# Kernel tuning notes

Hardware: AMD Instinct MI355X
Metric: run time of the kernel (lower is better)

## Reference

```python
import jax, jax.numpy as jnp
import numpy as np

B, S = 4096, 256
D = 32  # output_size // 4


def setup_inputs() -> dict:
    key = jax.random.key(0)
    ks = jax.random.split(key, 32)
    # continuous features
    cont_p = jax.random.normal(ks[0], (B, S, 3), dtype=jnp.float32)
    cont_c = jax.random.normal(ks[1], (B, S, 2), dtype=jnp.float32)
    # categorical features, per-column vocab sizes from Embedding tables
    vocabs_p = [2, 2, 2, 11, 34]
    cat_p = jnp.stack([
        jax.random.randint(ks[2 + i], (B, S), 0, v, dtype=jnp.int32)
        for i, v in enumerate(vocabs_p)], axis=2)
    vocabs_c = [19, 31]
    cat_c = jnp.stack([
        jax.random.randint(ks[7 + i], (B, S), 0, v, dtype=jnp.int32)
        for i, v in enumerate(vocabs_c)], axis=2)
    lengths = jax.random.randint(ks[9], (B,), 1, S + 1, dtype=jnp.int32)

    def lin(k, fan_in, fan_out):
        bound = 1.0 / np.sqrt(fan_in)
        kw, kb = jax.random.split(k)
        w = jax.random.uniform(kw, (fan_in, fan_out), jnp.float32, -bound, bound)
        b = jax.random.uniform(kb, (fan_out,), jnp.float32, -bound, bound)
        return w, b

    w_p1, b_p1 = lin(ks[10], 3, D)
    w_p2, b_p2 = lin(ks[11], D, D)
    w_c1, b_c1 = lin(ks[12], 2, D)
    w_c2, b_c2 = lin(ks[13], D, D)
    emb_gender = jax.random.normal(ks[14], (2, D), dtype=jnp.float32)
    emb_korean = jax.random.normal(ks[15], (2, D), dtype=jnp.float32)
    emb_primary = jax.random.normal(ks[16], (2, D), dtype=jnp.float32)
    emb_job = jax.random.normal(ks[17], (11, D), dtype=jnp.float32)
    emb_rep = jax.random.normal(ks[18], (34, D), dtype=jnp.float32)
    emb_place = jax.random.normal(ks[19], (19, D), dtype=jnp.float32)
    emb_add = jax.random.normal(ks[20], (31, D), dtype=jnp.float32)
    w_fc1, b_fc1 = lin(ks[21], 128, 64)
    w_fc2, b_fc2 = lin(ks[22], 64, 2)

    return dict(cont_p=cont_p, cont_c=cont_c, cat_p=cat_p, cat_c=cat_c,
                lengths=lengths,
                w_p1=w_p1, b_p1=b_p1, w_p2=w_p2, b_p2=b_p2,
                w_c1=w_c1, b_c1=b_c1, w_c2=w_c2, b_c2=b_c2,
                emb_gender=emb_gender, emb_korean=emb_korean,
                emb_primary=emb_primary, emb_job=emb_job, emb_rep=emb_rep,
                emb_place=emb_place, emb_add=emb_add,
                w_fc1=w_fc1, b_fc1=b_fc1, w_fc2=w_fc2, b_fc2=b_fc2)


def reference(cont_p, cont_c, cat_p, cat_c, lengths,
              w_p1, b_p1, w_p2, b_p2, w_c1, b_c1, w_c2, b_c2,
              emb_gender, emb_korean, emb_primary, emb_job, emb_rep,
              emb_place, emb_add, w_fc1, b_fc1, w_fc2, b_fc2):
    # small per-token MLPs on continuous features -> [B,S,D]
    hp = jax.nn.relu(cont_p @ w_p1 + b_p1) @ w_p2 + b_p2
    hc = jax.nn.relu(cont_c @ w_c1 + b_c1) @ w_c2 + b_c2
    # multi-table embedding lookups, averaged per group -> [B,S,D]
    ep = (emb_gender[cat_p[:, :, 0]] + emb_korean[cat_p[:, :, 1]] +
          emb_primary[cat_p[:, :, 2]] + emb_job[cat_p[:, :, 3]] +
          emb_rep[cat_p[:, :, 4]]) / 5.0
    ec = (emb_place[cat_c[:, :, 0]] + emb_add[cat_c[:, :, 1]]) / 2.0
    # concat order matches torch: (cat_p, cat_c, cont_p, cont_c) -> [B,S,128]
    x = jnp.concatenate([ep, ec, hp, hc], axis=2)
    # ragged mean pool over first lengths[i] positions (masked segment mean)
    mask = (jnp.arange(x.shape[1])[None, :] < lengths[:, None])
    pooled = jnp.sum(x * mask[:, :, None], axis=1) / lengths[:, None].astype(x.dtype)
    # head: relu(fc1) -> relu(fc2); dropout p=0.0 is identity
    h = jax.nn.relu(pooled @ w_fc1 + b_fc1)
    return jax.nn.relu(h @ w_fc2 + b_fc2)
```

## Files before the change

### kernel.cpp

```cpp
#include <hip/hip_runtime.h>


#define BDIM 64

__global__ __launch_bounds__(BDIM)
void mlpreg_kernel(const float* __restrict__ cont_p,
                   const float* __restrict__ cont_c,
                   const int* __restrict__ cat_p,
                   const int* __restrict__ cat_c,
                   const int* __restrict__ lengths,
                   const float* __restrict__ w_p1, const float* __restrict__ b_p1,
                   const float* __restrict__ w_p2, const float* __restrict__ b_p2,
                   const float* __restrict__ w_c1, const float* __restrict__ b_c1,
                   const float* __restrict__ w_c2, const float* __restrict__ b_c2,
                   const float* __restrict__ emb_g,  const float* __restrict__ emb_k,
                   const float* __restrict__ emb_pr, const float* __restrict__ emb_j,
                   const float* __restrict__ emb_r,  const float* __restrict__ emb_pl,
                   const float* __restrict__ emb_a,
                   const float* __restrict__ w_fc1, const float* __restrict__ b_fc1,
                   const float* __restrict__ w_fc2, const float* __restrict__ b_fc2,
                   float* __restrict__ out)
{
    constexpr int S = 256;
    __shared__ float sP4[S * 4];
    __shared__ float sC2[S * 2];
    __shared__ int   hist[96];
    __shared__ float sPacc[64];
    __shared__ float sPooled[128];

    const int lane = threadIdx.x;
    const int b    = blockIdx.x;
    int L = lengths[b];
    if (L < 1) L = 1;
    if (L > S) L = S;
    const float invL = 1.0f / (float)L;
    const float Lf   = (float)L;

    const int*   kp = cat_p  + (size_t)b * (S * 5);
    const int*   kc = cat_c  + (size_t)b * (S * 2);
    const float* gp = cont_p + (size_t)b * (S * 3);
    const float* gc = cont_c + (size_t)b * (S * 2);

    hist[lane] = 0;
    if (lane < 32) hist[64 + lane] = 0;
    __syncthreads();

    for (int t = lane; t < L; t += BDIM) {
        float c0 = gp[t * 3 + 0], c1 = gp[t * 3 + 1], c2 = gp[t * 3 + 2];
        float4 v; v.x = c0; v.y = c1; v.z = c2; v.w = 0.f;
        *(float4*)&sP4[t * 4] = v;
        float2 u = *(const float2*)(gc + t * 2);
        *(float2*)&sC2[t * 2] = u;
    }

    int sg = 0, sk = 0, spr = 0;
    for (int i = lane; i < 5 * L; i += BDIM) {
        int v = kp[i];
        int col = i % 5;
        if      (col == 0) sg  += v;
        else if (col == 1) sk  += v;
        else if (col == 2) spr += v;
        else if (col == 3) atomicAdd(&hist[v], 1);
        else               atomicAdd(&hist[11 + v], 1);
    }
    for (int i = lane; i < 2 * L; i += BDIM) {
        int v = kc[i];
        atomicAdd(&hist[(i & 1) ? (64 + v) : (45 + v)], 1);
    }
    #pragma unroll
    for (int d = 32; d; d >>= 1) {
        sg  += __shfl_xor(sg,  d);
        sk  += __shfl_xor(sk,  d);
        spr += __shfl_xor(spr, d);
    }
    __syncthreads();

    const int pr = lane >> 5, ch = lane & 31;
    const float wp0 = w_p1[ch], wp1 = w_p1[32 + ch], wp2 = w_p1[64 + ch], bp = b_p1[ch];
    const float wc0 = w_c1[ch], wc1 = w_c1[32 + ch], bc = b_c1[ch];

    float accP = 0.f, accC = 0.f;
    #pragma unroll 4
    for (int t = pr; t < L; t += 2) {
        float4 cp = *(const float4*)&sP4[t * 4];
        float2 cc = *(const float2*)&sC2[t * 2];
        accP += fmaxf(fmaf(cp.x, wp0, fmaf(cp.y, wp1, fmaf(cp.z, wp2, bp))), 0.f);
        accC += fmaxf(fmaf(cc.x, wc0, fmaf(cc.y, wc1, bc)), 0.f);
    }
    accP += __shfl_down(accP, 32);
    accC += __shfl_down(accC, 32);
    if (lane < 32) {
        sPacc[ch]      = accP * invL;
        sPacc[32 + ch] = accC * invL;
    }

    if (pr == 0) {
        float cg = (float)sg, ck = (float)sk, cp = (float)spr;
        float s0 = fmaf(Lf - cg, emb_g[ch],  fmaf(cg, emb_g[32 + ch],
                   fmaf(Lf - ck, emb_k[ch],  ck * emb_k[32 + ch])));
        float s1 = fmaf(Lf - cp, emb_pr[ch], cp * emb_pr[32 + ch]);
        #pragma unroll
        for (int r = 0; r < 11; ++r) s0 = fmaf((float)hist[r],      emb_j[r * 32 + ch], s0);
        #pragma unroll
        for (int r = 0; r < 34; r += 2) {
            s0 = fmaf((float)hist[11 + r],     emb_r[(r + 0) * 32 + ch], s0);
            s1 = fmaf((float)hist[11 + r + 1], emb_r[(r + 1) * 32 + ch], s1);
        }
        sPooled[ch] = (s0 + s1) * (invL * 0.2f);
    } else {
        float s0 = 0.f, s1 = 0.f;
        #pragma unroll
        for (int r = 0; r < 19; ++r) s0 = fmaf((float)hist[45 + r], emb_pl[r * 32 + ch], s0);
        #pragma unroll
        for (int r = 0; r < 31; r += 2) {
            s0 = fmaf((float)hist[64 + r], emb_a[(r + 0) * 32 + ch], s0);
            if (r + 1 < 31)
                s1 = fmaf((float)hist[64 + r + 1], emb_a[(r + 1) * 32 + ch], s1);
        }
        sPooled[32 + ch] = (s0 + s1) * (invL * 0.5f);
    }
    __syncthreads();

    if (pr == 0) {
        float v0 = b_p2[ch], v1 = 0.f;
        #pragma unroll
        for (int k = 0; k < 32; k += 2) {
            v0 = fmaf(sPacc[k],     w_p2[(k + 0) * 32 + ch], v0);
            v1 = fmaf(sPacc[k + 1], w_p2[(k + 1) * 32 + ch], v1);
        }
        sPooled[64 + ch] = v0 + v1;
    } else {
        float v0 = b_c2[ch], v1 = 0.f;
        #pragma unroll
        for (int k = 0; k < 32; k += 2) {
            v0 = fmaf(sPacc[32 + k],     w_c2[(k + 0) * 32 + ch], v0);
            v1 = fmaf(sPacc[32 + k + 1], w_c2[(k + 1) * 32 + ch], v1);
        }
        sPooled[96 + ch] = v0 + v1;
    }
    __syncthreads();

    const float* wk = w_fc1 + lane;
    float v0 = b_fc1[lane], v1 = 0.f, v2 = 0.f, v3 = 0.f;
    #pragma unroll 8
    for (int k = 0; k < 128; k += 4) {
        float4 x = *(const float4*)&sPooled[k];
        v0 = fmaf(x.x, wk[(size_t)(k + 0) * 64], v0);
        v1 = fmaf(x.y, wk[(size_t)(k + 1) * 64], v1);
        v2 = fmaf(x.z, wk[(size_t)(k + 2) * 64], v2);
        v3 = fmaf(x.w, wk[(size_t)(k + 3) * 64], v3);
    }
    float h = fmaxf((v0 + v1) + (v2 + v3), 0.f);

    float p0 = h * w_fc2[lane * 2 + 0];
    float p1 = h * w_fc2[lane * 2 + 1];
    #pragma unroll
    for (int d = 32; d; d >>= 1) {
        p0 += __shfl_xor(p0, d);
        p1 += __shfl_xor(p1, d);
    }
    if (lane == 0) {
        float2 o;
        o.x = fmaxf(p0 + b_fc2[0], 0.f);
        o.y = fmaxf(p1 + b_fc2[1], 0.f);
        *(float2*)&out[(size_t)b * 2] = o;
    }
}

extern "C" void kernel_launch(void* const* d_in, const int* in_sizes, int n_in,
                              void* d_out, int out_size, void* d_ws, size_t ws_size,
                              hipStream_t stream) {
    const float* cont_p = (const float*)d_in[0];
    const float* cont_c = (const float*)d_in[1];
    const int*   cat_p  = (const int*)d_in[2];
    const int*   cat_c  = (const int*)d_in[3];
    const int*   lens   = (const int*)d_in[4];
    const float* w_p1   = (const float*)d_in[5];
    const float* b_p1   = (const float*)d_in[6];
    const float* w_p2   = (const float*)d_in[7];
    const float* b_p2   = (const float*)d_in[8];
    const float* w_c1   = (const float*)d_in[9];
    const float* b_c1   = (const float*)d_in[10];
    const float* w_c2   = (const float*)d_in[11];
    const float* b_c2   = (const float*)d_in[12];
    const float* emb_g  = (const float*)d_in[13];
    const float* emb_k  = (const float*)d_in[14];
    const float* emb_pr = (const float*)d_in[15];
    const float* emb_j  = (const float*)d_in[16];
    const float* emb_r  = (const float*)d_in[17];
    const float* emb_pl = (const float*)d_in[18];
    const float* emb_a  = (const float*)d_in[19];
    const float* w_fc1  = (const float*)d_in[20];
    const float* b_fc1  = (const float*)d_in[21];
    const float* w_fc2  = (const float*)d_in[22];
    const float* b_fc2  = (const float*)d_in[23];
    float* out = (float*)d_out;

    const int B = 4096;
    hipLaunchKernelGGL(mlpreg_kernel, dim3(B), dim3(BDIM), 0, stream,
                       cont_p, cont_c, cat_p, cat_c, lens,
                       w_p1, b_p1, w_p2, b_p2, w_c1, b_c1, w_c2, b_c2,
                       emb_g, emb_k, emb_pr, emb_j, emb_r, emb_pl, emb_a,
                       w_fc1, b_fc1, w_fc2, b_fc2, out);
}
```

Before: 144.9 us.

## Compute per-token MLP in registers per lane and reduce across the wave with transposed shuffles

Each lane now owns up to four tokens and accumulates all 32 hidden channels of both first-layer MLPs in registers. A butterfly transpose-reduce across the wave then produces the per-channel pooled sums. This replaces the shared-memory staging of continuous features and one barrier. Categorical columns are read per token in a single pass: the three binary columns are packed into one integer for the shuffle reduction, and all histogram updates are merged into one loop. The aim is to expose more independent memory loads and cut shared-memory round trips, at the cost of many more live registers and redundant weight loads per lane.

```diff
diff --git a/kernel.cpp b/kernel.cpp
--- a/kernel.cpp
+++ b/kernel.cpp
@@ -3,7 +3,67 @@
 
 #define BDIM 64
 
-__global__ __launch_bounds__(BDIM)
+__device__ __forceinline__ float wave_sum64(float v) {
+    #pragma unroll
+    for (int d = 32; d; d >>= 1) v += __shfl_xor(v, d);
+    return v;
+}
+
+__device__ __forceinline__ float transpose_reduce32(const float a[32], int lane) {
+    float x16[16];
+    {
+        const bool s = (lane & 16) != 0;
+        #pragma unroll
+        for (int i = 0; i < 16; ++i) {
+            float keep = s ? a[16 + i] : a[i];
+            float send = s ? a[i] : a[16 + i];
+            x16[i] = keep + __shfl_xor(send, 16);
+        }
+    }
+    float x8[8];
+    {
+        const bool s = (lane & 8) != 0;
+        #pragma unroll
+        for (int i = 0; i < 8; ++i) {
+            float keep = s ? x16[8 + i] : x16[i];
+            float send = s ? x16[i] : x16[8 + i];
+            x8[i] = keep + __shfl_xor(send, 8);
+        }
+    }
+    float x4[4];
+    {
+        const bool s = (lane & 4) != 0;
+        #pragma unroll
+        for (int i = 0; i < 4; ++i) {
+            float keep = s ? x8[4 + i] : x8[i];
+            float send = s ? x8[i] : x8[4 + i];
+            x4[i] = keep + __shfl_xor(send, 4);
+        }
+    }
+    float x2[2];
+    {
+        const bool s = (lane & 2) != 0;
+        #pragma unroll
+        for (int i = 0; i < 2; ++i) {
+            float keep = s ? x2[0] * 0.f + x4[2 + i] : x4[i];
+            (void)keep;
+            float k2 = s ? x4[2 + i] : x4[i];
+            float send = s ? x4[i] : x4[2 + i];
+            x2[i] = k2 + __shfl_xor(send, 2);
+        }
+    }
+    float v;
+    {
+        const bool s = (lane & 1) != 0;
+        float keep = s ? x2[1] : x2[0];
+        float send = s ? x2[0] : x2[1];
+        v = keep + __shfl_xor(send, 1);
+    }
+    v += __shfl_xor(v, 32);
+    return v;
+}
+
+__global__ __launch_bounds__(BDIM, 4)
 void mlpreg_kernel(const float* __restrict__ cont_p,
                    const float* __restrict__ cont_c,
                    const int* __restrict__ cat_p,
@@ -22,148 +82,178 @@
                    float* __restrict__ out)
 {
     constexpr int S = 256;
-    __shared__ float sP4[S * 4];
-    __shared__ float sC2[S * 2];
     __shared__ int   hist[96];
     __shared__ float sPacc[64];
-    __shared__ float sPooled[128];
+    __shared__ __align__(16) float sPool[128];
 
     const int lane = threadIdx.x;
     const int b    = blockIdx.x;
     int L = lengths[b];
-    if (L < 1) L = 1;
-    if (L > S) L = S;
-    const float invL = 1.0f / (float)L;
-    const float Lf   = (float)L;
-
+    L = (L < 1) ? 1 : (L > S ? S : L);
+    const float Lf = (float)L, invL = 1.0f / Lf;
+
+    hist[lane] = 0;
+    if (lane < 32) hist[64 + lane] = 0;
+
+    const int ch = lane & 31, h = lane >> 5;
+    const float* gp = cont_p + (size_t)b * (S * 3);
+    const float* gc = cont_c + (size_t)b * (S * 2);
     const int*   kp = cat_p  + (size_t)b * (S * 5);
     const int*   kc = cat_c  + (size_t)b * (S * 2);
-    const float* gp = cont_p + (size_t)b * (S * 3);
-    const float* gc = cont_c + (size_t)b * (S * 2);
-
-    hist[lane] = 0;
-    if (lane < 32) hist[64 + lane] = 0;
+
+    const int t0 = lane, t1 = 64 + lane;
+    const int i0 = (t0 < L) ? t0 : (L - 1);
+    const int i1 = (t1 < L) ? t1 : (L - 1);
+    const float m0 = (t0 < L) ? 1.f : 0.f;
+    const float m1 = (t1 < L) ? 1.f : 0.f;
+    float a00 = gp[3 * i0], a01 = gp[3 * i0 + 1], a02 = gp[3 * i0 + 2];
+    float2 e0 = *(const float2*)&gc[2 * i0];
+    float a10 = gp[3 * i1], a11 = gp[3 * i1 + 1], a12 = gp[3 * i1 + 2];
+    float2 e1 = *(const float2*)&gc[2 * i1];
+
+    int pk = 0;
+    #pragma unroll
+    for (int blk = 0; blk < 4; ++blk) {
+        if (L > blk * 64) {
+            int t = blk * 64 + lane;
+            if (t < L) {
+                int v0 = kp[5 * t], v1 = kp[5 * t + 1], v2 = kp[5 * t + 2],
+                    v3 = kp[5 * t + 3], v4 = kp[5 * t + 4];
+                int2 q = *(const int2*)&kc[2 * t];
+                pk += v0 + (v1 << 10) + (v2 << 20);
+                atomicAdd(&hist[v3], 1);
+                atomicAdd(&hist[11 + v4], 1);
+                atomicAdd(&hist[46 + q.x], 1);
+                atomicAdd(&hist[65 + q.y], 1);
+            }
+        }
+    }
+    #pragma unroll
+    for (int d = 32; d; d >>= 1) pk += __shfl_xor(pk, d);
+    const float sg = (float)(pk & 1023), sk = (float)((pk >> 10) & 1023),
+                sp = (float)(pk >> 20);
+
+    float AP[32], AC[32];
+    #pragma unroll
+    for (int j = 0; j < 32; ++j) {
+        float vp = fmaf(a00, w_p1[j], fmaf(a01, w_p1[32 + j], fmaf(a02, w_p1[64 + j], b_p1[j])));
+        AP[j] = m0 * fmaxf(vp, 0.f);
+        float vc = fmaf(e0.x, w_c1[j], fmaf(e0.y, w_c1[32 + j], b_c1[j]));
+        AC[j] = m0 * fmaxf(vc, 0.f);
+    }
+    if (L > 64) {
+        #pragma unroll
+        for (int j = 0; j < 32; ++j) {
+            float vp = fmaf(a10, w_p1[j], fmaf(a11, w_p1[32 + j], fmaf(a12, w_p1[64 + j], b_p1[j])));
+            AP[j] = fmaf(m1, fmaxf(vp, 0.f), AP[j]);
+            float vc = fmaf(e1.x, w_c1[j], fmaf(e1.y, w_c1[32 + j], b_c1[j]));
+            AC[j] = fmaf(m1, fmaxf(vc, 0.f), AC[j]);
+        }
+    }
+    if (L > 128) {
+        int t = 128 + lane;
+        int ti = (t < L) ? t : (L - 1);
+        float m = (t < L) ? 1.f : 0.f;
+        float c0 = gp[3 * ti], c1 = gp[3 * ti + 1], c2 = gp[3 * ti + 2];
+        float2 dd = *(const float2*)&gc[2 * ti];
+        #pragma unroll
+        for (int j = 0; j < 32; ++j) {
+            float vp = fmaf(c0, w_p1[j], fmaf(c1, w_p1[32 + j], fmaf(c2, w_p1[64 + j], b_p1[j])));
+            AP[j] = fmaf(m, fmaxf(vp, 0.f), AP[j]);
+            float vc = fmaf(dd.x, w_c1[j], fmaf(dd.y, w_c1[32 + j], b_c1[j]));
+            AC[j] = fmaf(m, fmaxf(vc, 0.f), AC[j]);
+        }
+    }
+    if (L > 192) {
+        int t = 192 + lane;
+        int ti = (t < L) ? t : (L - 1);
+        float m = (t < L) ? 1.f : 0.f;
+        float c0 = gp[3 * ti], c1 = gp[3 * ti + 1], c2 = gp[3 * ti + 2];
+        float2 dd = *(const float2*)&gc[2 * ti];
+        #pragma unroll
+        for (int j = 0; j < 32; ++j) {
+            float vp = fmaf(c0, w_p1[j], fmaf(c1, w_p1[32 + j], fmaf(c2, w_p1[64 + j], b_p1[j])));
+            AP[j] = fmaf(m, fmaxf(vp, 0.f), AP[j]);
+            float vc = fmaf(dd.x, w_c1[j], fmaf(dd.y, w_c1[32 + j], b_c1[j]));
+            AC[j] = fmaf(m, fmaxf(vc, 0.f), AC[j]);
+        }
+    }
+
+    float paccP = transpose_reduce32(AP, lane);
+    float paccC = transpose_reduce32(AC, lane);
+    if (lane < 32) {
+        sPacc[ch]      = paccP * invL;
+        sPacc[32 + ch] = paccC * invL;
+    }
     __syncthreads();
 
-    for (int t = lane; t < L; t += BDIM) {
-        float c0 = gp[t * 3 + 0], c1 = gp[t * 3 + 1], c2 = gp[t * 3 + 2];
-        float4 v; v.x = c0; v.y = c1; v.z = c2; v.w = 0.f;
-        *(float4*)&sP4[t * 4] = v;
-        float2 u = *(const float2*)(gc + t * 2);
-        *(float2*)&sC2[t * 2] = u;
-    }
-
-    int sg = 0, sk = 0, spr = 0;
-    for (int i = lane; i < 5 * L; i += BDIM) {
-        int v = kp[i];
-        int col = i % 5;
-        if      (col == 0) sg  += v;
-        else if (col == 1) sk  += v;
-        else if (col == 2) spr += v;
-        else if (col == 3) atomicAdd(&hist[v], 1);
-        else               atomicAdd(&hist[11 + v], 1);
-    }
-    for (int i = lane; i < 2 * L; i += BDIM) {
-        int v = kc[i];
-        atomicAdd(&hist[(i & 1) ? (64 + v) : (45 + v)], 1);
-    }
-    #pragma unroll
-    for (int d = 32; d; d >>= 1) {
-        sg  += __shfl_xor(sg,  d);
-        sk  += __shfl_xor(sk,  d);
-        spr += __shfl_xor(spr, d);
+    float vp0 = h ? 0.f : b_p2[ch];
+    #pragma unroll
+    for (int i = 0; i < 16; ++i) {
+        int k = h * 16 + i;
+        vp0 = fmaf(sPacc[k], w_p2[k * 32 + ch], vp0);
+    }
+    vp0 += __shfl_down(vp0, 32);
+    float vc0 = h ? 0.f : b_c2[ch];
+    #pragma unroll
+    for (int i = 0; i < 16; ++i) {
+        int k = h * 16 + i;
+        vc0 = fmaf(sPacc[32 + k], w_c2[k * 32 + ch], vc0);
+    }
+    vc0 += __shfl_down(vc0, 32);
+
+    float ep = 0.f;
+    if (h == 0) {
+        ep  = fmaf(Lf - sg, emb_g[ch],  sg * emb_g[32 + ch]);
+        ep += fmaf(Lf - sk, emb_k[ch],  sk * emb_k[32 + ch]);
+        ep += fmaf(Lf - sp, emb_pr[ch], sp * emb_pr[32 + ch]);
+    }
+    #pragma unroll
+    for (int i = 0; i < 23; ++i) {
+        int bb = 2 * i + h;
+        int cnt = hist[bb];
+        int br = (bb < 44) ? bb : 44;
+        const float* tp = (bb < 11) ? (emb_j + bb * 32) : (emb_r + (br - 11) * 32);
+        ep = fmaf((float)cnt, tp[ch], ep);
+    }
+    ep += __shfl_down(ep, 32);
+    float ec = 0.f;
+    #pragma unroll
+    for (int i = 0; i < 25; ++i) {
+        int bb = 46 + 2 * i + h;
+        int cnt = hist[bb];
+        const float* tp = (bb < 65) ? (emb_pl + (bb - 46) * 32) : (emb_a + (bb - 65) * 32);
+        ec = fmaf((float)cnt, tp[ch], ec);
+    }
+    ec += __shfl_down(ec, 32);
+
+    if (lane < 32) {
+        sPool[ch]      = ep * (invL * 0.2f);
+        sPool[32 + ch] = ec * (invL * 0.5f);
+        sPool[64 + ch] = vp0;
+        sPool[96 + ch] = vc0;
     }
     __syncthreads();
 
-    const int pr = lane >> 5, ch = lane & 31;
-    const float wp0 = w_p1[ch], wp1 = w_p1[32 + ch], wp2 = w_p1[64 + ch], bp = b_p1[ch];
-    const float wc0 = w_c1[ch], wc1 = w_c1[32 + ch], bc = b_c1[ch];
-
-    float accP = 0.f, accC = 0.f;
-    #pragma unroll 4
-    for (int t = pr; t < L; t += 2) {
-        float4 cp = *(const float4*)&sP4[t * 4];
-        float2 cc = *(const float2*)&sC2[t * 2];
-        accP += fmaxf(fmaf(cp.x, wp0, fmaf(cp.y, wp1, fmaf(cp.z, wp2, bp))), 0.f);
-        accC += fmaxf(fmaf(cc.x, wc0, fmaf(cc.y, wc1, bc)), 0.f);
-    }
-    accP += __shfl_down(accP, 32);
-    accC += __shfl_down(accC, 32);
-    if (lane < 32) {
-        sPacc[ch]      = accP * invL;
-        sPacc[32 + ch] = accC * invL;
-    }
-
-    if (pr == 0) {
-        float cg = (float)sg, ck = (float)sk, cp = (float)spr;
-        float s0 = fmaf(Lf - cg, emb_g[ch],  fmaf(cg, emb_g[32 + ch],
-                   fmaf(Lf - ck, emb_k[ch],  ck * emb_k[32 + ch])));
-        float s1 = fmaf(Lf - cp, emb_pr[ch], cp * emb_pr[32 + ch]);
-        #pragma unroll
-        for (int r = 0; r < 11; ++r) s0 = fmaf((float)hist[r],      emb_j[r * 32 + ch], s0);
-        #pragma unroll
-        for (int r = 0; r < 34; r += 2) {
-            s0 = fmaf((float)hist[11 + r],     emb_r[(r + 0) * 32 + ch], s0);
-            s1 = fmaf((float)hist[11 + r + 1], emb_r[(r + 1) * 32 + ch], s1);
-        }
-        sPooled[ch] = (s0 + s1) * (invL * 0.2f);
-    } else {
-        float s0 = 0.f, s1 = 0.f;
-        #pragma unroll
-        for (int r = 0; r < 19; ++r) s0 = fmaf((float)hist[45 + r], emb_pl[r * 32 + ch], s0);
-        #pragma unroll
-        for (int r = 0; r < 31; r += 2) {
-            s0 = fmaf((float)hist[64 + r], emb_a[(r + 0) * 32 + ch], s0);
-            if (r + 1 < 31)
-                s1 = fmaf((float)hist[64 + r + 1], emb_a[(r + 1) * 32 + ch], s1);
-        }
-        sPooled[32 + ch] = (s0 + s1) * (invL * 0.5f);
-    }
-    __syncthreads();
-
-    if (pr == 0) {
-        float v0 = b_p2[ch], v1 = 0.f;
-        #pragma unroll
-        for (int k = 0; k < 32; k += 2) {
-            v0 = fmaf(sPacc[k],     w_p2[(k + 0) * 32 + ch], v0);
-            v1 = fmaf(sPacc[k + 1], w_p2[(k + 1) * 32 + ch], v1);
-        }
-        sPooled[64 + ch] = v0 + v1;
-    } else {
-        float v0 = b_c2[ch], v1 = 0.f;
-        #pragma unroll
-        for (int k = 0; k < 32; k += 2) {
-            v0 = fmaf(sPacc[32 + k],     w_c2[(k + 0) * 32 + ch], v0);
-            v1 = fmaf(sPacc[32 + k + 1], w_c2[(k + 1) * 32 + ch], v1);
-        }
-        sPooled[96 + ch] = v0 + v1;
-    }
-    __syncthreads();
-
-    const float* wk = w_fc1 + lane;
-    float v0 = b_fc1[lane], v1 = 0.f, v2 = 0.f, v3 = 0.f;
-    #pragma unroll 8
-    for (int k = 0; k < 128; k += 4) {
-        float4 x = *(const float4*)&sPooled[k];
-        v0 = fmaf(x.x, wk[(size_t)(k + 0) * 64], v0);
-        v1 = fmaf(x.y, wk[(size_t)(k + 1) * 64], v1);
-        v2 = fmaf(x.z, wk[(size_t)(k + 2) * 64], v2);
-        v3 = fmaf(x.w, wk[(size_t)(k + 3) * 64], v3);
-    }
-    float h = fmaxf((v0 + v1) + (v2 + v3), 0.f);
-
-    float p0 = h * w_fc2[lane * 2 + 0];
-    float p1 = h * w_fc2[lane * 2 + 1];
-    #pragma unroll
-    for (int d = 32; d; d >>= 1) {
-        p0 += __shfl_xor(p0, d);
-        p1 += __shfl_xor(p1, d);
-    }
+    float q0 = b_fc1[lane], q1 = 0.f, q2 = 0.f, q3 = 0.f;
+    #pragma unroll
+    for (int k4 = 0; k4 < 32; ++k4) {
+        float4 x = *(const float4*)&sPool[4 * k4];
+        q0 = fmaf(x.x, w_fc1[(size_t)(4 * k4 + 0) * 64 + lane], q0);
+        q1 = fmaf(x.y, w_fc1[(size_t)(4 * k4 + 1) * 64 + lane], q1);
+        q2 = fmaf(x.z, w_fc1[(size_t)(4 * k4 + 2) * 64 + lane], q2);
+        q3 = fmaf(x.w, w_fc1[(size_t)(4 * k4 + 3) * 64 + lane], q3);
+    }
+    float hv = fmaxf((q0 + q1) + (q2 + q3), 0.f);
+
+    float2 wf = *(const float2*)&w_fc2[2 * lane];
+    float p0 = wave_sum64(hv * wf.x);
+    float p1 = wave_sum64(hv * wf.y);
     if (lane == 0) {
-        float2 o;
-        o.x = fmaxf(p0 + b_fc2[0], 0.f);
-        o.y = fmaxf(p1 + b_fc2[1], 0.f);
-        *(float2*)&out[(size_t)b * 2] = o;
+        float2 o2;
+        o2.x = fmaxf(p0 + b_fc2[0], 0.f);
+        o2.y = fmaxf(p1 + b_fc2[1], 0.f);
+        *(float2*)&out[(size_t)b * 2] = o2;
     }
 }
 
@@ -196,8 +286,7 @@
     const float* b_fc2  = (const float*)d_in[23];
     float* out = (float*)d_out;
 
-    const int B = 4096;
-    hipLaunchKernelGGL(mlpreg_kernel, dim3(B), dim3(BDIM), 0, stream,
+    hipLaunchKernelGGL(mlpreg_kernel, dim3(4096), dim3(BDIM), 0, stream,
                        cont_p, cont_c, cat_p, cat_c, lens,
                        w_p1, b_p1, w_p2, b_p2, w_c1, b_c1, w_c2, b_c2,
                        emb_g, emb_k, emb_pr, emb_j, emb_r, emb_pl, emb_a,
```

Measured after the change: 162.4 us. 12.1% more time.
